# Performance work log

Measured on AMD Instinct MI355X. Metric: run time of the kernel, lower is better.

## Reference

```python
import jax, jax.numpy as jnp
import numpy as np

B, T, D, U = 64, 2048, 256, 256

def setup_inputs() -> dict:
    key = jax.random.key(0)
    ks = jax.random.split(key, 8)
    return {
        "query": jax.random.normal(ks[0], (B, D), dtype=jnp.float32),
        "values": jax.random.normal(ks[1], (B, T, D), dtype=jnp.float32),
        "W1_w": jax.random.normal(ks[2], (D, U), dtype=jnp.float32) * 0.05,
        "W1_b": jnp.zeros((U,), dtype=jnp.float32),
        "W2_w": jax.random.normal(ks[3], (D, U), dtype=jnp.float32) * 0.05,
        "W2_b": jnp.zeros((U,), dtype=jnp.float32),
        "V_w": jax.random.normal(ks[4], (U, 1), dtype=jnp.float32) * 0.05,
        "V_b": jnp.zeros((1,), dtype=jnp.float32),
    }

def reference(query, values, W1_w, W1_b, W2_w, W2_b, V_w, V_b):
    # query: [B, D] -> [B, 1, U]
    q_proj = (query @ W1_w + W1_b)[:, None, :]
    # values: [B, T, D] -> [B, T, U]
    v_proj = jnp.einsum('btd,du->btu', values, W2_w) + W2_b
    # score: [B, T, 1]
    score = jnp.tanh(q_proj + v_proj) @ V_w + V_b
    attention_weights = jax.nn.softmax(score, axis=1)  # over time axis
    context_vector = jnp.sum(attention_weights * values, axis=1)  # [B, D]
    return (context_vector, attention_weights)
```

## Files before the change

kernel.cpp:

```cpp
#include <hip/hip_runtime.h>
#include <stdint.h>

#define B_ 64
#define T_ 2048
#define D_ 256
#define U_ 256
#define BT 128
#define NT (BT / 16)
#define TC (T_ / BT)
#define SHIFT_ 8.0f

typedef _Float16 half8   __attribute__((ext_vector_type(8)));
typedef float    floatx4 __attribute__((ext_vector_type(4)));

typedef const __attribute__((address_space(1))) void cg_void;
typedef __attribute__((address_space(3))) void       ls_void;

__global__ void prep_kernel(const float* __restrict__ query,
                            const float* __restrict__ W1_w,
                            const float* __restrict__ W1_b,
                            const float* __restrict__ W2_b,
                            const float* __restrict__ W2_w,
                            float* __restrict__ qb,
                            _Float16* __restrict__ w2t) {
    __shared__ float qrow[D_];
    __shared__ float tile[32][33];
    if (blockIdx.x < 64) {
        const int b = blockIdx.x;
        const int u = threadIdx.x;
        qrow[u] = query[b * D_ + u];
        __syncthreads();
        float a0 = 0.f, a1 = 0.f, a2 = 0.f, a3 = 0.f;
#pragma unroll 4
        for (int d = 0; d < D_; d += 4) {
            a0 += qrow[d    ] * W1_w[(d    ) * U_ + u];
            a1 += qrow[d + 1] * W1_w[(d + 1) * U_ + u];
            a2 += qrow[d + 2] * W1_w[(d + 2) * U_ + u];
            a3 += qrow[d + 3] * W1_w[(d + 3) * U_ + u];
        }
        qb[b * U_ + u] = (a0 + a1) + (a2 + a3) + W1_b[u] + W2_b[u];
    } else {
        const int bid = blockIdx.x - 64;
        const int tu = bid & 7;
        const int td = bid >> 3;
        const int c  = threadIdx.x & 31;
        const int r0 = threadIdx.x >> 5;
#pragma unroll
        for (int i = 0; i < 4; ++i) {
            int r = r0 + i * 8;
            tile[r][c] = W2_w[(td * 32 + r) * U_ + tu * 32 + c];
        }
        __syncthreads();
#pragma unroll
        for (int i = 0; i < 4; ++i) {
            int r = r0 + i * 8;
            w2t[(tu * 32 + r) * D_ + td * 32 + c] = (_Float16)tile[c][r];
        }
    }
}

__launch_bounds__(256, 2)
__global__ void score_ctx_kernel(const float* __restrict__ values,
                                 const _Float16* __restrict__ w2t,
                                 const float* __restrict__ qb,
                                 const float* __restrict__ V_w,
                                 float* __restrict__ scores,
                                 float* __restrict__ pctx,
                                 float* __restrict__ pl) {
    __shared__ __align__(16) float buf[2][16 * D_];
    __shared__ __align__(16) float s_part2[16][4];
    __shared__ float sbuf[BT];

    const int b     = blockIdx.y;
    const int chunk = blockIdx.x;
    const int tid   = threadIdx.x;
    const int wave  = tid >> 6;
    const int lane  = tid & 63;
    const int n16   = lane & 15;
    const int quad  = lane >> 4;
    const int u0    = wave * 64;

    half8 bfrag[4][8];
#pragma unroll
    for (int ut = 0; ut < 4; ++ut) {
        const int u = u0 + ut * 16 + n16;
#pragma unroll
        for (int k = 0; k < 8; ++k)
            bfrag[ut][k] = *(const half8*)(w2t + u * D_ + k * 32 + quad * 8);
    }
    float qbv[4], vwv[4];
#pragma unroll
    for (int ut = 0; ut < 4; ++ut) {
        const int u = u0 + ut * 16 + n16;
        qbv[ut] = qb[b * U_ + u];
        vwv[ut] = V_w[u];
    }

    const float* vbase = values + (size_t)b * T_ * D_ + (size_t)chunk * BT * D_;

    const int e0 = (quad * 2) ^ (n16 & 7);
    const int e1 = e0 ^ 1;

    const int g = tid >> 2, lo = tid & 3;
    int co[8];
#pragma unroll
    for (int s = 0; s < 8; ++s) co[s] = (((g ^ s) & 63) << 2) + lo;

    float c = 0.f;
    float l = 0.f;

    auto stage = [&](int tile, int bi) {
        const float* src = vbase + tile * 16 * D_;
#pragma unroll
        for (int i = 0; i < 4; ++i) {
            const int r = i * 4 + wave;
            const float* gp = src + r * D_ + ((lane ^ (r & 7)) << 2);
            float* lp = &buf[bi][r * D_];
            __builtin_amdgcn_global_load_lds((cg_void*)gp, (ls_void*)lp, 16, 0, 0);
        }
    };

    stage(0, 0);

#pragma unroll 1
    for (int tile = 0; tile < NT; ++tile) {
        const int cur = tile & 1;
        asm volatile("s_waitcnt vmcnt(0) lgkmcnt(0)" ::: "memory");
        __builtin_amdgcn_s_barrier();
        asm volatile("" ::: "memory");

        if (tile + 1 < NT) stage(tile + 1, cur ^ 1);

        const float* a0p = &buf[cur][n16 * D_] + (e0 << 2);
        const float* a1p = &buf[cur][n16 * D_] + (e1 << 2);
        floatx4 acc[4] = {};
#pragma unroll
        for (int k = 0; k < 8; ++k) {
            floatx4 q0 = *(const floatx4*)(a0p + (k << 5));
            floatx4 q1 = *(const floatx4*)(a1p + (k << 5));
            half8 a;
            a[0] = (_Float16)q0.x; a[1] = (_Float16)q0.y;
            a[2] = (_Float16)q0.z; a[3] = (_Float16)q0.w;
            a[4] = (_Float16)q1.x; a[5] = (_Float16)q1.y;
            a[6] = (_Float16)q1.z; a[7] = (_Float16)q1.w;
#pragma unroll
            for (int ut = 0; ut < 4; ++ut)
                acc[ut] = __builtin_amdgcn_mfma_f32_16x16x32_f16(a, bfrag[ut][k], acc[ut], 0, 0, 0);
        }

        float part[4];
#pragma unroll
        for (int r = 0; r < 4; ++r) {
            float sa = 0.f;
#pragma unroll
            for (int ut = 0; ut < 4; ++ut) {
                float x  = acc[ut][r] + qbv[ut];
                float e  = __expf(2.f * x);
                float th = 1.f - __fdividef(2.f, e + 1.f);
                sa += th * vwv[ut];
            }
            part[r] = sa;
        }
#pragma unroll
        for (int m = 1; m < 16; m <<= 1)
#pragma unroll
            for (int r = 0; r < 4; ++r)
                part[r] += __shfl_xor(part[r], m, 16);
        if (n16 == 0) {
#pragma unroll
            for (int r = 0; r < 4; ++r)
                s_part2[quad * 4 + r][wave] = part[r];
        }

        asm volatile("s_waitcnt lgkmcnt(0)" ::: "memory");
        __builtin_amdgcn_s_barrier();
        asm volatile("" ::: "memory");

        const float* bufp = &buf[cur][0];
        const float* sp2  = &s_part2[0][0];
#pragma unroll
        for (int t = 0; t < 16; ++t) {
            floatx4 sp = *(const floatx4*)(sp2 + t * 4);
            float sv = (sp.x + sp.y) + (sp.z + sp.w);
            float w  = __expf(sv - SHIFT_);
            l += w;
            c += w * bufp[t * D_ + co[t & 7]];
        }
        if (tid < 16) {
            floatx4 sp = *(const floatx4*)(sp2 + tid * 4);
            sbuf[tile * 16 + tid] = (sp.x + sp.y) + (sp.z + sp.w);
        }
    }

    __syncthreads();
    pctx[(b * TC + chunk) * D_ + tid] = c;
    if (tid < BT) scores[b * T_ + chunk * BT + tid] = sbuf[tid];
    if (tid == 0) pl[b * TC + chunk] = l;
}

__global__ void finalize_kernel(const float* __restrict__ pctx,
                                const float* __restrict__ pl,
                                const float* __restrict__ scores,
                                float* __restrict__ ctx,
                                float* __restrict__ attn) {
    const int b = blockIdx.x, tid = threadIdx.x;
    float L = 0.f;
#pragma unroll
    for (int i = 0; i < TC; ++i) L += pl[b * TC + i];
    float s = 0.f;
#pragma unroll
    for (int i = 0; i < TC; ++i) s += pctx[(b * TC + i) * D_ + tid];
    const float invL = __fdividef(1.f, L);
    ctx[b * D_ + tid] = s * invL;
#pragma unroll
    for (int j = 0; j < T_ / 256; ++j) {
        const int t = j * 256 + tid;
        attn[b * T_ + t] = __expf(scores[b * T_ + t] - SHIFT_) * invL;
    }
}

extern "C" void kernel_launch(void* const* d_in, const int* in_sizes, int n_in,
                              void* d_out, int out_size, void* d_ws, size_t ws_size,
                              hipStream_t stream) {
    const float* query  = (const float*)d_in[0];
    const float* values = (const float*)d_in[1];
    const float* W1_w   = (const float*)d_in[2];
    const float* W1_b   = (const float*)d_in[3];
    const float* W2_w   = (const float*)d_in[4];
    const float* W2_b   = (const float*)d_in[5];
    const float* V_w    = (const float*)d_in[6];

    float* out  = (float*)d_out;
    float* ctx  = out;
    float* attn = out + B_ * D_;

    char* ws = (char*)d_ws;
    float*    qb     = (float*)ws;
    _Float16* w2t    = (_Float16*)(ws + (64 << 10));
    float*    scores = (float*)(ws + (192 << 10));
    float*    pctx   = (float*)(ws + (704 << 10));
    float*    pl     = (float*)(ws + (1728 << 10));

    prep_kernel     <<<dim3(128),     dim3(256), 0, stream>>>(query, W1_w, W1_b, W2_b, W2_w, qb, w2t);
    score_ctx_kernel<<<dim3(TC, B_),  dim3(256), 0, stream>>>(values, w2t, qb, V_w, scores, pctx, pl);
    finalize_kernel <<<dim3(B_),      dim3(256), 0, stream>>>(pctx, pl, scores, ctx, attn);
}
```

Before: 240.0 us.

## Process two 16-row tiles per iteration with deeper LDS buffering and larger chunks

Doubles the time chunk per block to 256 rows and processes two 16-row tiles per loop iteration, with four LDS buffers so two tiles are prefetched while two are computed. This halves the number of barriers per row and interleaves two independent MFMA accumulation chains for more ILP. It also switches the f32-to-f16 conversion to packed cvt_pkrtz, which rounds toward zero rather than to nearest. In exchange, LDS use doubles to about 64KB per block, which may limit occupancy, and the grid halves to 512 blocks, reducing parallelism.

```diff
diff --git a/kernel.cpp b/kernel.cpp
--- a/kernel.cpp
+++ b/kernel.cpp
@@ -5,12 +5,14 @@
 #define T_ 2048
 #define D_ 256
 #define U_ 256
-#define BT 128
+#define BT 256
 #define NT (BT / 16)
+#define NP (NT / 2)
 #define TC (T_ / BT)
 #define SHIFT_ 8.0f
 
 typedef _Float16 half8   __attribute__((ext_vector_type(8)));
+typedef __fp16   fp16x2  __attribute__((ext_vector_type(2)));
 typedef float    floatx4 __attribute__((ext_vector_type(4)));
 
 typedef const __attribute__((address_space(1))) void cg_void;
@@ -67,8 +69,8 @@
                                  float* __restrict__ scores,
                                  float* __restrict__ pctx,
                                  float* __restrict__ pl) {
-    __shared__ __align__(16) float buf[2][16 * D_];
-    __shared__ __align__(16) float s_part2[16][4];
+    __shared__ __align__(16) float buf[4][16 * D_];
+    __shared__ __align__(16) float s_part2[2][16][4];
     __shared__ float sbuf[BT];
 
     const int b     = blockIdx.y;
@@ -88,6 +90,7 @@
         for (int k = 0; k < 8; ++k)
             bfrag[ut][k] = *(const half8*)(w2t + u * D_ + k * 32 + quad * 8);
     }
+
     float qbv[4], vwv[4];
 #pragma unroll
     for (int ut = 0; ut < 4; ++ut) {
@@ -106,8 +109,8 @@
 #pragma unroll
     for (int s = 0; s < 8; ++s) co[s] = (((g ^ s) & 63) << 2) + lo;
 
-    float c = 0.f;
-    float l = 0.f;
+    float c0a = 0.f, c1a = 0.f;
+    float l0a = 0.f, l1a = 0.f;
 
     auto stage = [&](int tile, int bi) {
         const float* src = vbase + tile * 16 * D_;
@@ -121,81 +124,102 @@
     };
 
     stage(0, 0);
+    stage(1, 1);
 
 #pragma unroll 1
-    for (int tile = 0; tile < NT; ++tile) {
-        const int cur = tile & 1;
+    for (int i = 0; i < NP; ++i) {
+        const int s0 = (i & 1) << 1;
         asm volatile("s_waitcnt vmcnt(0) lgkmcnt(0)" ::: "memory");
         __builtin_amdgcn_s_barrier();
         asm volatile("" ::: "memory");
 
-        if (tile + 1 < NT) stage(tile + 1, cur ^ 1);
-
-        const float* a0p = &buf[cur][n16 * D_] + (e0 << 2);
-        const float* a1p = &buf[cur][n16 * D_] + (e1 << 2);
-        floatx4 acc[4] = {};
+        if (i + 1 < NP) { stage(2 * i + 2, s0 ^ 2); stage(2 * i + 3, (s0 ^ 2) + 1); }
+
+        const float* base0 = &buf[s0][n16 * D_];
+        const float* base1 = &buf[s0 + 1][n16 * D_];
+        floatx4 acc0[4] = {};
+        floatx4 acc1[4] = {};
 #pragma unroll
         for (int k = 0; k < 8; ++k) {
-            floatx4 q0 = *(const floatx4*)(a0p + (k << 5));
-            floatx4 q1 = *(const floatx4*)(a1p + (k << 5));
-            half8 a;
-            a[0] = (_Float16)q0.x; a[1] = (_Float16)q0.y;
-            a[2] = (_Float16)q0.z; a[3] = (_Float16)q0.w;
-            a[4] = (_Float16)q1.x; a[5] = (_Float16)q1.y;
-            a[6] = (_Float16)q1.z; a[7] = (_Float16)q1.w;
-#pragma unroll
-            for (int ut = 0; ut < 4; ++ut)
-                acc[ut] = __builtin_amdgcn_mfma_f32_16x16x32_f16(a, bfrag[ut][k], acc[ut], 0, 0, 0);
-        }
-
-        float part[4];
+            floatx4 q00 = *(const floatx4*)(base0 + (e0 << 2) + (k << 5));
+            floatx4 q01 = *(const floatx4*)(base0 + (e1 << 2) + (k << 5));
+            floatx4 q10 = *(const floatx4*)(base1 + (e0 << 2) + (k << 5));
+            floatx4 q11 = *(const floatx4*)(base1 + (e1 << 2) + (k << 5));
+            union { fp16x2 h2[4]; half8 h8; } ua, ub;
+            ua.h2[0] = __builtin_amdgcn_cvt_pkrtz(q00.x, q00.y);
+            ua.h2[1] = __builtin_amdgcn_cvt_pkrtz(q00.z, q00.w);
+            ua.h2[2] = __builtin_amdgcn_cvt_pkrtz(q01.x, q01.y);
+            ua.h2[3] = __builtin_amdgcn_cvt_pkrtz(q01.z, q01.w);
+            ub.h2[0] = __builtin_amdgcn_cvt_pkrtz(q10.x, q10.y);
+            ub.h2[1] = __builtin_amdgcn_cvt_pkrtz(q10.z, q10.w);
+            ub.h2[2] = __builtin_amdgcn_cvt_pkrtz(q11.x, q11.y);
+            ub.h2[3] = __builtin_amdgcn_cvt_pkrtz(q11.z, q11.w);
+#pragma unroll
+            for (int ut = 0; ut < 4; ++ut) {
+                acc0[ut] = __builtin_amdgcn_mfma_f32_16x16x32_f16(ua.h8, bfrag[ut][k], acc0[ut], 0, 0, 0);
+                acc1[ut] = __builtin_amdgcn_mfma_f32_16x16x32_f16(ub.h8, bfrag[ut][k], acc1[ut], 0, 0, 0);
+            }
+        }
+
+        float part0[4], part1[4];
 #pragma unroll
         for (int r = 0; r < 4; ++r) {
-            float sa = 0.f;
+            float sa = 0.f, sb = 0.f;
 #pragma unroll
             for (int ut = 0; ut < 4; ++ut) {
-                float x  = acc[ut][r] + qbv[ut];
-                float e  = __expf(2.f * x);
-                float th = 1.f - __fdividef(2.f, e + 1.f);
-                sa += th * vwv[ut];
-            }
-            part[r] = sa;
+                float x0 = acc0[ut][r] + qbv[ut];
+                float x1 = acc1[ut][r] + qbv[ut];
+                float e0v = __expf(2.f * x0);
+                float e1v = __expf(2.f * x1);
+                sa += (1.f - __fdividef(2.f, e0v + 1.f)) * vwv[ut];
+                sb += (1.f - __fdividef(2.f, e1v + 1.f)) * vwv[ut];
+            }
+            part0[r] = sa; part1[r] = sb;
         }
 #pragma unroll
         for (int m = 1; m < 16; m <<= 1)
 #pragma unroll
-            for (int r = 0; r < 4; ++r)
-                part[r] += __shfl_xor(part[r], m, 16);
+            for (int r = 0; r < 4; ++r) {
+                part0[r] += __shfl_xor(part0[r], m, 16);
+                part1[r] += __shfl_xor(part1[r], m, 16);
+            }
         if (n16 == 0) {
 #pragma unroll
-            for (int r = 0; r < 4; ++r)
-                s_part2[quad * 4 + r][wave] = part[r];
+            for (int r = 0; r < 4; ++r) {
+                s_part2[0][quad * 4 + r][wave] = part0[r];
+                s_part2[1][quad * 4 + r][wave] = part1[r];
+            }
         }
 
         asm volatile("s_waitcnt lgkmcnt(0)" ::: "memory");
         __builtin_amdgcn_s_barrier();
         asm volatile("" ::: "memory");
 
-        const float* bufp = &buf[cur][0];
-        const float* sp2  = &s_part2[0][0];
+        const float* sp2 = &s_part2[0][0][0];
+        const float* v0  = &buf[s0][0];
 #pragma unroll
         for (int t = 0; t < 16; ++t) {
-            floatx4 sp = *(const floatx4*)(sp2 + t * 4);
-            float sv = (sp.x + sp.y) + (sp.z + sp.w);
-            float w  = __expf(sv - SHIFT_);
-            l += w;
-            c += w * bufp[t * D_ + co[t & 7]];
-        }
-        if (tid < 16) {
-            floatx4 sp = *(const floatx4*)(sp2 + tid * 4);
-            sbuf[tile * 16 + tid] = (sp.x + sp.y) + (sp.z + sp.w);
+            floatx4 spA = *(const floatx4*)(sp2 + t * 4);
+            floatx4 spB = *(const floatx4*)(sp2 + 64 + t * 4);
+            float svA = (spA.x + spA.y) + (spA.z + spA.w);
+            float svB = (spB.x + spB.y) + (spB.z + spB.w);
+            float wA = __expf(svA - SHIFT_);
+            float wB = __expf(svB - SHIFT_);
+            l0a += wA; l1a += wB;
+            c0a += wA * v0[t * D_ + co[t & 7]];
+            c1a += wB * v0[16 * D_ + t * D_ + co[t & 7]];
+        }
+        if (tid < 32) {
+            const int p = tid >> 4, r = tid & 15;
+            floatx4 sp = *(const floatx4*)(sp2 + p * 64 + r * 4);
+            sbuf[i * 32 + tid] = (sp.x + sp.y) + (sp.z + sp.w);
         }
     }
 
     __syncthreads();
-    pctx[(b * TC + chunk) * D_ + tid] = c;
-    if (tid < BT) scores[b * T_ + chunk * BT + tid] = sbuf[tid];
-    if (tid == 0) pl[b * TC + chunk] = l;
+    pctx[(b * TC + chunk) * D_ + tid] = c0a + c1a;
+    scores[b * T_ + chunk * BT + tid] = sbuf[tid];
+    if (tid == 0) pl[b * TC + chunk] = l0a + l1a;
 }
 
 __global__ void finalize_kernel(const float* __restrict__ pctx,
@@ -239,7 +263,7 @@
     _Float16* w2t    = (_Float16*)(ws + (64 << 10));
     float*    scores = (float*)(ws + (192 << 10));
     float*    pctx   = (float*)(ws + (704 << 10));
-    float*    pl     = (float*)(ws + (1728 << 10));
+    float*    pl     = (float*)(ws + (1216 << 10));
 
     prep_kernel     <<<dim3(128),     dim3(256), 0, stream>>>(query, W1_w, W1_b, W2_b, W2_w, qb, w2t);
     score_ctx_kernel<<<dim3(TC, B_),  dim3(256), 0, stream>>>(values, w2t, qb, V_w, scores, pctx, pl);
```

After: 272.3 us. 1.13x slower.
